# Optimization experiments

Measured on AMD Instinct MI355X. Metric: run time of the kernel, lower is better.

## Reference

```python
import jax, jax.numpy as jnp
import numpy as np

B, H, S, D, R = 2, 16, 2048, 64, 64  # batch, heads, seq, head_dim, R_features


def setup_inputs() -> dict:
    key = jax.random.key(0)
    ks = jax.random.split(key, 5)
    query = jax.random.normal(ks[0], (B, H, S, D), jnp.float32)
    keys = jax.random.normal(ks[1], (B, H, S, D), jnp.float32)
    vals = jax.random.normal(ks[2], (B, H, S, D), jnp.float32)
    # causal mask; masked_fill(mask == 0, -inf)
    mask = jnp.tril(jnp.ones((S, S), jnp.int32))[None, None]
    # LazyLinear(R) params: weight [D, R] (stored pre-transposed), bias [R]
    W = jax.random.normal(ks[3], (D, R), jnp.float32) / np.float32(np.sqrt(D))
    b = jax.random.normal(ks[4], (R,), jnp.float32) * 0.02
    return {"query": query, "keys": keys, "vals": vals, "mask": mask, "W": W, "b": b}


def reference(query, keys, vals, mask, W, b):
    d = query.shape[-1]
    r = W.shape[-1]
    # random-feature projections
    Wq = query @ W + b            # [B,H,S,R]
    Wk = keys @ W + b             # [B,H,S,R]
    phi_q = jnp.concatenate([jnp.cos(Wq), jnp.sin(Wq)], axis=-1)  # [B,H,S,2R]
    phi_k = jnp.concatenate([jnp.cos(Wk), jnp.sin(Wk)], axis=-1)
    energy = jnp.einsum("bhqr,bhkr->bhqk", phi_q, phi_k) / r      # [B,H,S,S]
    energy = energy * energy
    preattn = jnp.log(energy + 1e-5)
    # magnitude term: (||q||_2^2 + ||k||_2^2) / (2*sqrt(d))
    qn = jnp.sum(query * query, axis=-1, keepdims=True)           # [B,H,S,1]
    kn = jnp.sum(keys * keys, axis=-1, keepdims=True)             # [B,H,S,1]
    preattn = preattn + (qn + jnp.swapaxes(kn, -2, -1)) / (2.0 * d ** 0.5)
    preattn = jnp.where(mask == 0, -jnp.inf, preattn)
    attn = jax.nn.softmax(preattn, axis=-1)
    # dropout is identity in eval mode
    return attn @ vals  # [B,H,S,D]
```

## Files before the change

### kernel.cpp

```cpp
#include <hip/hip_runtime.h>
#include <hip/hip_fp16.h>

#define SEQ 2048
#define NBH 32
#define C1f 0.09016844005556021f

typedef _Float16 f16x8 __attribute__((ext_vector_type(8)));
typedef __fp16 fp16x2 __attribute__((ext_vector_type(2)));
typedef float f32x4 __attribute__((ext_vector_type(4)));
typedef __attribute__((address_space(1))) const unsigned GASU;
typedef __attribute__((address_space(3))) unsigned LASU;

union U16 { fp16x2 h[4]; f16x8 v; };

__device__ __forceinline__ void gll16(const void* g, void* l) {
  __builtin_amdgcn_global_load_lds((GASU*)g, (LASU*)l, 16, 0, 0);
}

__global__ __launch_bounds__(256) void prep(
    const float* __restrict__ qg, const float* __restrict__ kg,
    const float* __restrict__ vg, const float* __restrict__ Wg,
    const float* __restrict__ bg,
    __half* __restrict__ phiq, __half* __restrict__ phik,
    __half* __restrict__ vt, float* __restrict__ ckn) {
  __shared__ __align__(16) float smem[64 * 68 + 64 * 64];
  const int x = blockIdx.x;
  const int tid = threadIdx.x;
  if (x >= 2048) {
    const int i = x - 2048;
    const int bh = i >> 5, s0 = (i & 31) * 64;
    float* t = smem;
    const float* base = vg + ((long)bh * SEQ + s0) * 64;
    #pragma unroll
    for (int i2 = 0; i2 < 4; ++i2) {
      int seg = i2 * 256 + tid;
      int srow = seg >> 4, sc4 = (seg & 15) << 2;
      float4 xv = *(const float4*)(base + srow * 64 + sc4);
      t[srow * 65 + sc4 + 0] = xv.x; t[srow * 65 + sc4 + 1] = xv.y;
      t[srow * 65 + sc4 + 2] = xv.z; t[srow * 65 + sc4 + 3] = xv.w;
    }
    __syncthreads();
    int d = tid >> 2, sc = (tid & 3) << 4;
    __half tmp[16];
    #pragma unroll
    for (int j = 0; j < 16; ++j) tmp[j] = __float2half(t[(sc + j) * 65 + d]);
    __half* dst = vt + ((long)bh * 64 + d) * SEQ + s0 + sc;
    *(uint4*)dst = *(uint4*)&tmp[0];
    *(uint4*)(dst + 8) = *(uint4*)&tmp[8];
    return;
  }
  const int wave = tid >> 6, lane = tid & 63;
  const int g = lane >> 4, ql = lane & 15;
  const int isk = x >= 1024;
  const long rowblk = (long)(x & 1023) * 64;
  const float* src = isk ? kg : qg;
  __half* dphi = isk ? phik : phiq;
  float* w_l = smem;
  float* x_l = smem + 64 * 68;

  #pragma unroll
  for (int i2 = 0; i2 < 4; ++i2) {
    int seg = i2 * 256 + tid;
    int d = seg >> 4, rc = (seg & 15) << 2;
    float4 wv = *(const float4*)(Wg + d * 64 + rc);
    w_l[(rc + 0) * 68 + d] = wv.x; w_l[(rc + 1) * 68 + d] = wv.y;
    w_l[(rc + 2) * 68 + d] = wv.z; w_l[(rc + 3) * 68 + d] = wv.w;
  }
  const float* xb = src + rowblk * 64;
  #pragma unroll
  for (int i2 = 0; i2 < 4; ++i2) {
    int seg = i2 * 256 + tid;
    int row = seg >> 4;
    int off = ((seg & 15) * 4) ^ ((row & 7) << 2);
    gll16(xb + row * 64 + off, &x_l[seg * 4]);
  }
  float bias[4];
  #pragma unroll
  for (int rt = 0; rt < 4; ++rt) bias[rt] = bg[rt * 16 + ql];
  __syncthreads();

  f16x8 bh_[2][4], bl_[2][4];
  #pragma unroll
  for (int rt = 0; rt < 4; ++rt)
    #pragma unroll
    for (int ks = 0; ks < 2; ++ks) {
      f32x4 wa = *(const f32x4*)&w_l[(rt * 16 + ql) * 68 + ks * 32 + g * 8];
      f32x4 wb = *(const f32x4*)&w_l[(rt * 16 + ql) * 68 + ks * 32 + g * 8 + 4];
      #pragma unroll
      for (int j = 0; j < 4; ++j) {
        float w0 = wa[j]; _Float16 h0 = (_Float16)w0;
        bh_[ks][rt][j] = h0; bl_[ks][rt][j] = (_Float16)(w0 - (float)h0);
        float w1 = wb[j]; _Float16 h1 = (_Float16)w1;
        bh_[ks][rt][4 + j] = h1; bl_[ks][rt][4 + j] = (_Float16)(w1 - (float)h1);
      }
    }

  const int rl = wave * 16 + ql;
  float xv[16];
  #pragma unroll
  for (int ks = 0; ks < 2; ++ks)
    #pragma unroll
    for (int h = 0; h < 2; ++h) {
      int fi = (rl * 64 + ks * 32 + g * 8 + h * 4) ^ ((ql & 7) << 2);
      f32x4 u = *(const f32x4*)&x_l[fi];
      #pragma unroll
      for (int j = 0; j < 4; ++j) xv[ks * 8 + h * 4 + j] = u[j];
    }
  float nn = 0.f;
  #pragma unroll
  for (int j = 0; j < 16; ++j) nn = fmaf(xv[j], xv[j], nn);
  nn += __shfl_xor(nn, 16);
  nn += __shfl_xor(nn, 32);
  if (isk && g == 0) ckn[rowblk + rl] = 1e-5f * exp2f(nn * C1f);
  float scl = isk ? exp2f(nn * (C1f * 0.5f)) * 0.125f : 0.125f;
  float s4[4];
  #pragma unroll
  for (int i2 = 0; i2 < 4; ++i2) s4[i2] = __shfl(scl, (lane & 48) | (g * 4 + i2));

  f16x8 ah[2], al[2];
  #pragma unroll
  for (int ks = 0; ks < 2; ++ks)
    #pragma unroll
    for (int j = 0; j < 8; ++j) {
      float v = xv[ks * 8 + j];
      _Float16 hv = (_Float16)v;
      ah[ks][j] = hv;
      al[ks][j] = (_Float16)(v - (float)hv);
    }
  f32x4 sacc[4] = {};
  #pragma unroll
  for (int ks = 0; ks < 2; ++ks)
    #pragma unroll
    for (int rt = 0; rt < 4; ++rt) {
      sacc[rt] = __builtin_amdgcn_mfma_f32_16x16x32_f16(ah[ks], bh_[ks][rt], sacc[rt], 0, 0, 0);
      sacc[rt] = __builtin_amdgcn_mfma_f32_16x16x32_f16(al[ks], bh_[ks][rt], sacc[rt], 0, 0, 0);
      sacc[rt] = __builtin_amdgcn_mfma_f32_16x16x32_f16(ah[ks], bl_[ks][rt], sacc[rt], 0, 0, 0);
    }
  #pragma unroll
  for (int rt = 0; rt < 4; ++rt)
    #pragma unroll
    for (int i2 = 0; i2 < 4; ++i2) {
      float wq = sacc[rt][i2] + bias[rt];
      float sv, cv;
      __sincosf(wq, &sv, &cv);
      long row = rowblk + wave * 16 + g * 4 + i2;
      dphi[row * 128 + rt * 16 + ql] = __float2half(cv * s4[i2]);
      dphi[row * 128 + 64 + rt * 16 + ql] = __float2half(sv * s4[i2]);
    }
}

__global__ __launch_bounds__(256, 3) void attn_kernel(
    const __half* __restrict__ phiq_g, const __half* __restrict__ phik_g,
    const __half* __restrict__ vt_g, const float* __restrict__ ckn_g,
    float* __restrict__ out) {
  const int x = blockIdx.x;
  const int bh = ((x & 7) << 2) | ((x >> 3) & 3);
  const int u = (x >> 5) & 7;
  const int slot = x >> 8;
  const int s = (slot == 0) ? 31 - u : (slot == 1) ? 16 + u : (slot == 2) ? 15 - u : u;
  const int tid = threadIdx.x;
  const int wv = tid >> 6, lane = tid & 63;
  const int g = lane >> 4, ql = lane & 15;
  const int qh = wv & 1, kh = wv >> 1;
  const long rowbase = (long)bh * SEQ;
  const int qbase = s * 64 + qh * 32;

  __shared__ __align__(16) char smem[49152];
  __half* phik_l = (__half*)smem;
  __half* vt_l = (__half*)(smem + 32768);

  const __half* pkb = phik_g + rowbase * 128;
  const __half* vtb = vt_g + (long)bh * 64 * SEQ;
  const float* ckp = ckn_g + rowbase + kh * 32 + g * 8;

  unsigned koffv[4], kdstv[4], voffv[2], vdstv[2];
  #pragma unroll
  for (int i = 0; i < 4; ++i) {
    int seg = i * 256 + tid;
    int rho = seg >> 4;
    int sg = (rho & 32) | ((rho & 12) << 1) | ((rho & 16) >> 2) | (rho & 3);
    int off = ((seg & 15) * 8) ^ ((rho & 15) << 3);
    koffv[i] = sg * 128 + off;
    kdstv[i] = seg * 8;
  }
  #pragma unroll
  for (int i = 0; i < 2; ++i) {
    int seg = i * 256 + tid;
    int d = seg >> 3;
    int off = ((seg & 7) * 8) ^ ((d & 7) << 3);
    voffv[i] = d * SEQ + off;
    vdstv[i] = seg * 8;
  }

  auto stageKV = [&](int tn, int bb) {
    const __half* kb = pkb + (long)tn * 8192;
    #pragma unroll
    for (int i = 0; i < 4; ++i) gll16(kb + koffv[i], phik_l + bb * 8192 + kdstv[i]);
    const __half* vb = vtb + tn * 64;
    #pragma unroll
    for (int i = 0; i < 2; ++i) gll16(vb + voffv[i], vt_l + bb * 4096 + vdstv[i]);
  };

  stageKV(0, 0);

  f16x8 bq[2][4];
  #pragma unroll
  for (int c = 0; c < 2; ++c)
    #pragma unroll
    for (int ks = 0; ks < 4; ++ks)
      bq[c][ks] = *(const f16x8*)(phiq_g + (rowbase + qbase + c * 16 + ql) * 128 + ks * 32 + g * 8);

  float lsum[2] = {0.f, 0.f};
  f32x4 acc[2][4] = {};

  auto step = [&](int t, int bb) {
    asm volatile("s_waitcnt vmcnt(0)" ::: "memory");
    __builtin_amdgcn_s_barrier();
    __builtin_amdgcn_sched_barrier(0);

    const float* ckt = ckp + t * 64;
    f32x4 ckA = *(const f32x4*)(ckt);
    f32x4 ckB = *(const f32x4*)(ckt + 4);
    __builtin_amdgcn_sched_barrier(0);
    if (t < s) stageKV(t + 1, bb ^ 1);
    __builtin_amdgcn_sched_barrier(0);

    const bool skip = (qbase + 31) < (t * 64 + kh * 32);
    if (!skip) {
      f32x4 sS[2][2] = {};
      __builtin_amdgcn_s_setprio(1);
      #pragma unroll
      for (int ks = 0; ks < 4; ++ks) {
        int i0 = (bb * 8192 + (kh * 32 + ql) * 128 + ks * 32 + g * 8) ^ (ql << 3);
        int i1 = (bb * 8192 + (kh * 32 + 16 + ql) * 128 + ks * 32 + g * 8) ^ (ql << 3);
        f16x8 a0 = *(const f16x8*)&phik_l[i0];
        f16x8 a1 = *(const f16x8*)&phik_l[i1];
        sS[0][0] = __builtin_amdgcn_mfma_f32_16x16x32_f16(a0, bq[0][ks], sS[0][0], 0, 0, 0);
        sS[0][1] = __builtin_amdgcn_mfma_f32_16x16x32_f16(a1, bq[0][ks], sS[0][1], 0, 0, 0);
        sS[1][0] = __builtin_amdgcn_mfma_f32_16x16x32_f16(a0, bq[1][ks], sS[1][0], 0, 0, 0);
        sS[1][1] = __builtin_amdgcn_mfma_f32_16x16x32_f16(a1, bq[1][ks], sS[1][1], 0, 0, 0);
      }
      __builtin_amdgcn_s_setprio(0);

      f16x8 pa[2];
      #pragma unroll
      for (int c = 0; c < 2; ++c) {
        const int qrow = qbase + c * 16 + ql;
        const bool domask = (t * 64 + kh * 32 + 31) > (qbase + c * 16);
        float e[8];
        #pragma unroll
        for (int kt = 0; kt < 2; ++kt)
          #pragma unroll
          for (int r = 0; r < 4; ++r) {
            float dd = sS[c][kt][r];
            float pe = fmaf(dd, dd, kt ? ckB[r] : ckA[r]);
            if (domask) {
              int key = t * 64 + kh * 32 + g * 8 + kt * 4 + r;
              pe = (key <= qrow) ? pe : 0.f;
            }
            e[kt * 4 + r] = pe;
          }
        lsum[c] += ((e[0] + e[1]) + (e[2] + e[3])) + ((e[4] + e[5]) + (e[6] + e[7]));
        U16 A;
        A.h[0] = __builtin_amdgcn_cvt_pkrtz(e[0], e[1]);
        A.h[1] = __builtin_amdgcn_cvt_pkrtz(e[2], e[3]);
        A.h[2] = __builtin_amdgcn_cvt_pkrtz(e[4], e[5]);
        A.h[3] = __builtin_amdgcn_cvt_pkrtz(e[6], e[7]);
        pa[c] = A.v;
      }

      __builtin_amdgcn_s_setprio(1);
      #pragma unroll
      for (int dt = 0; dt < 4; ++dt) {
        int idx = (bb * 4096 + (dt * 16 + ql) * 64 + kh * 32 + g * 8) ^ ((ql & 7) << 3);
        f16x8 bv = *(const f16x8*)&vt_l[idx];
        acc[0][dt] = __builtin_amdgcn_mfma_f32_16x16x32_f16(pa[0], bv, acc[0][dt], 0, 0, 0);
        acc[1][dt] = __builtin_amdgcn_mfma_f32_16x16x32_f16(pa[1], bv, acc[1][dt], 0, 0, 0);
      }
      __builtin_amdgcn_s_setprio(0);
    }
  };

  for (int t = 0; t <= s; t += 2) {
    step(t, 0);
    if (t + 1 <= s) step(t + 1, 1);
  }

  float* dump = (float*)smem;
  __syncthreads();
  if (kh) {
    #pragma unroll
    for (int c = 0; c < 2; ++c) {
      #pragma unroll
      for (int dt = 0; dt < 4; ++dt)
        #pragma unroll
        for (int r = 0; r < 4; ++r)
          dump[(qh * 34 + c * 16 + dt * 4 + r) * 64 + lane] = acc[c][dt][r];
      dump[(qh * 34 + 32 + c) * 64 + lane] = lsum[c];
    }
  }
  __syncthreads();
  if (!kh) {
    #pragma unroll
    for (int c = 0; c < 2; ++c) {
      lsum[c] += dump[(qh * 34 + 32 + c) * 64 + lane];
      lsum[c] += __shfl_xor(lsum[c], 16);
      lsum[c] += __shfl_xor(lsum[c], 32);
      #pragma unroll
      for (int dt = 0; dt < 4; ++dt)
        #pragma unroll
        for (int r = 0; r < 4; ++r)
          acc[c][dt][r] += dump[(qh * 34 + c * 16 + dt * 4 + r) * 64 + lane];
    }
    #pragma unroll
    for (int c = 0; c < 2; ++c)
      #pragma unroll
      for (int r = 0; r < 4; ++r) {
        float ls = __shfl(lsum[c], (lane & 48) | (g * 4 + r));
        float inv = __builtin_amdgcn_rcpf(ls);
        float* o = out + (rowbase + qbase + c * 16 + g * 4 + r) * 64 + ql;
        #pragma unroll
        for (int dt = 0; dt < 4; ++dt) o[dt * 16] = acc[c][dt][r] * inv;
      }
  }
}

extern "C" void kernel_launch(void* const* d_in, const int* in_sizes, int n_in,
                              void* d_out, int out_size, void* d_ws, size_t ws_size,
                              hipStream_t stream) {
  const float* q = (const float*)d_in[0];
  const float* k = (const float*)d_in[1];
  const float* v = (const float*)d_in[2];
  const float* W = (const float*)d_in[4];
  const float* b = (const float*)d_in[5];
  float* out = (float*)d_out;

  char* ws = (char*)d_ws;
  __half* phiq = (__half*)ws;
  __half* phik = (__half*)(ws + 16777216);
  __half* vt = (__half*)(ws + 33554432);
  float* ckn = (float*)(ws + 41943040);

  prep<<<dim3(3072), 256, 0, stream>>>(q, k, v, W, b, phiq, phik, vt, ckn);
  attn_kernel<<<dim3(1024), 256, 0, stream>>>(phiq, phik, vt, ckn, out);
}
```

Baseline: 61.47 us.

## Compute query random features inside attention kernel instead of prep pass

Moves the phi_q projection (split-fp16 MFMA GEMM plus sincos) from the prep kernel into the attention kernel's prologue. The query tile is loaded into LDS and projected there, and the result is read back as MFMA operands. Prep now handles only keys, the V transpose, and one extra block that writes split-fp16 transposed W for the attention kernel to load. This removes the phi_q global write and re-read and cuts prep's block count. In exchange, the attention kernel gains a longer prologue with extra barriers and register pressure.

```diff
diff --git a/kernel.cpp b/kernel.cpp
--- a/kernel.cpp
+++ b/kernel.cpp
@@ -18,16 +18,30 @@
 }
 
 __global__ __launch_bounds__(256) void prep(
-    const float* __restrict__ qg, const float* __restrict__ kg,
-    const float* __restrict__ vg, const float* __restrict__ Wg,
-    const float* __restrict__ bg,
-    __half* __restrict__ phiq, __half* __restrict__ phik,
-    __half* __restrict__ vt, float* __restrict__ ckn) {
+    const float* __restrict__ kg, const float* __restrict__ vg,
+    const float* __restrict__ Wg, const float* __restrict__ bg,
+    __half* __restrict__ phik, __half* __restrict__ vt,
+    float* __restrict__ ckn, __half* __restrict__ wth, __half* __restrict__ wtl) {
   __shared__ __align__(16) float smem[64 * 68 + 64 * 64];
   const int x = blockIdx.x;
   const int tid = threadIdx.x;
-  if (x >= 2048) {
-    const int i = x - 2048;
+  if (x == 2048) {
+    int r = tid & 63, dg = tid >> 6;
+    __half th[16], tl[16];
+    #pragma unroll
+    for (int j = 0; j < 16; ++j) {
+      float w = Wg[(dg * 16 + j) * 64 + r];
+      th[j] = __float2half(w);
+      tl[j] = __float2half(w - __half2float(th[j]));
+    }
+    *(uint4*)&wth[r * 64 + dg * 16] = *(uint4*)&th[0];
+    *(uint4*)&wth[r * 64 + dg * 16 + 8] = *(uint4*)&th[8];
+    *(uint4*)&wtl[r * 64 + dg * 16] = *(uint4*)&tl[0];
+    *(uint4*)&wtl[r * 64 + dg * 16 + 8] = *(uint4*)&tl[8];
+    return;
+  }
+  if (x >= 1024) {
+    const int i = x - 1024;
     const int bh = i >> 5, s0 = (i & 31) * 64;
     float* t = smem;
     const float* base = vg + ((long)bh * SEQ + s0) * 64;
@@ -51,10 +65,7 @@
   }
   const int wave = tid >> 6, lane = tid & 63;
   const int g = lane >> 4, ql = lane & 15;
-  const int isk = x >= 1024;
-  const long rowblk = (long)(x & 1023) * 64;
-  const float* src = isk ? kg : qg;
-  __half* dphi = isk ? phik : phiq;
+  const long rowblk = (long)x * 64;
   float* w_l = smem;
   float* x_l = smem + 64 * 68;
 
@@ -66,7 +77,7 @@
     w_l[(rc + 0) * 68 + d] = wv.x; w_l[(rc + 1) * 68 + d] = wv.y;
     w_l[(rc + 2) * 68 + d] = wv.z; w_l[(rc + 3) * 68 + d] = wv.w;
   }
-  const float* xb = src + rowblk * 64;
+  const float* xb = kg + rowblk * 64;
   #pragma unroll
   for (int i2 = 0; i2 < 4; ++i2) {
     int seg = i2 * 256 + tid;
@@ -111,8 +122,8 @@
   for (int j = 0; j < 16; ++j) nn = fmaf(xv[j], xv[j], nn);
   nn += __shfl_xor(nn, 16);
   nn += __shfl_xor(nn, 32);
-  if (isk && g == 0) ckn[rowblk + rl] = 1e-5f * exp2f(nn * C1f);
-  float scl = isk ? exp2f(nn * (C1f * 0.5f)) * 0.125f : 0.125f;
+  if (g == 0) ckn[rowblk + rl] = 1e-5f * exp2f(nn * C1f);
+  float scl = exp2f(nn * (C1f * 0.5f)) * 0.125f;
   float s4[4];
   #pragma unroll
   for (int i2 = 0; i2 < 4; ++i2) s4[i2] = __shfl(scl, (lane & 48) | (g * 4 + i2));
@@ -144,15 +155,16 @@
       float sv, cv;
       __sincosf(wq, &sv, &cv);
       long row = rowblk + wave * 16 + g * 4 + i2;
-      dphi[row * 128 + rt * 16 + ql] = __float2half(cv * s4[i2]);
-      dphi[row * 128 + 64 + rt * 16 + ql] = __float2half(sv * s4[i2]);
+      phik[row * 128 + rt * 16 + ql] = __float2half(cv * s4[i2]);
+      phik[row * 128 + 64 + rt * 16 + ql] = __float2half(sv * s4[i2]);
     }
 }
 
 __global__ __launch_bounds__(256, 3) void attn_kernel(
-    const __half* __restrict__ phiq_g, const __half* __restrict__ phik_g,
+    const float* __restrict__ qg, const __half* __restrict__ phik_g,
     const __half* __restrict__ vt_g, const float* __restrict__ ckn_g,
-    float* __restrict__ out) {
+    const __half* __restrict__ wth, const __half* __restrict__ wtl,
+    const float* __restrict__ bg, float* __restrict__ out) {
   const int x = blockIdx.x;
   const int bh = ((x & 7) << 2) | ((x >> 3) & 3);
   const int u = (x >> 5) & 7;
@@ -173,6 +185,82 @@
   const __half* vtb = vt_g + (long)bh * 64 * SEQ;
   const float* ckp = ckn_g + rowbase + kh * 32 + g * 8;
 
+  f16x8 bq[2][4];
+  {
+    float* x_l = (float*)smem;
+    __half* phi_l = (__half*)smem + 8192;
+    const float* xb = qg + (rowbase + s * 64) * 64;
+    #pragma unroll
+    for (int i = 0; i < 4; ++i) {
+      int seg = i * 256 + tid;
+      int row = seg >> 4;
+      int off = ((seg & 15) * 4) ^ ((row & 7) << 2);
+      gll16(xb + row * 64 + off, &x_l[seg * 4]);
+    }
+    f16x8 bh_[2][4], bl_[2][4];
+    #pragma unroll
+    for (int rt = 0; rt < 4; ++rt)
+      #pragma unroll
+      for (int ks = 0; ks < 2; ++ks) {
+        bh_[ks][rt] = *(const f16x8*)&wth[(rt * 16 + ql) * 64 + ks * 32 + g * 8];
+        bl_[ks][rt] = *(const f16x8*)&wtl[(rt * 16 + ql) * 64 + ks * 32 + g * 8];
+      }
+    float bias[4];
+    #pragma unroll
+    for (int rt = 0; rt < 4; ++rt) bias[rt] = bg[rt * 16 + ql];
+    asm volatile("s_waitcnt vmcnt(0)" ::: "memory");
+    __builtin_amdgcn_s_barrier();
+
+    const int rl = wv * 16 + ql;
+    float xv[16];
+    #pragma unroll
+    for (int ks = 0; ks < 2; ++ks)
+      #pragma unroll
+      for (int h = 0; h < 2; ++h) {
+        int fi = (rl * 64 + ks * 32 + g * 8 + h * 4) ^ ((ql & 7) << 2);
+        f32x4 uu = *(const f32x4*)&x_l[fi];
+        #pragma unroll
+        for (int j = 0; j < 4; ++j) xv[ks * 8 + h * 4 + j] = uu[j];
+      }
+    f16x8 ah[2], al[2];
+    #pragma unroll
+    for (int ks = 0; ks < 2; ++ks)
+      #pragma unroll
+      for (int j = 0; j < 8; ++j) {
+        float v = xv[ks * 8 + j];
+        _Float16 hv = (_Float16)v;
+        ah[ks][j] = hv;
+        al[ks][j] = (_Float16)(v - (float)hv);
+      }
+    f32x4 sacc[4] = {};
+    #pragma unroll
+    for (int ks = 0; ks < 2; ++ks)
+      #pragma unroll
+      for (int rt = 0; rt < 4; ++rt) {
+        sacc[rt] = __builtin_amdgcn_mfma_f32_16x16x32_f16(ah[ks], bh_[ks][rt], sacc[rt], 0, 0, 0);
+        sacc[rt] = __builtin_amdgcn_mfma_f32_16x16x32_f16(al[ks], bh_[ks][rt], sacc[rt], 0, 0, 0);
+        sacc[rt] = __builtin_amdgcn_mfma_f32_16x16x32_f16(ah[ks], bl_[ks][rt], sacc[rt], 0, 0, 0);
+      }
+    #pragma unroll
+    for (int rt = 0; rt < 4; ++rt)
+      #pragma unroll
+      for (int i2 = 0; i2 < 4; ++i2) {
+        float wq = sacc[rt][i2] + bias[rt];
+        float sv, cv;
+        __sincosf(wq, &sv, &cv);
+        int row = wv * 16 + g * 4 + i2;
+        phi_l[row * 128 + rt * 16 + ql] = __float2half(cv * 0.125f);
+        phi_l[row * 128 + 64 + rt * 16 + ql] = __float2half(sv * 0.125f);
+      }
+    __syncthreads();
+    #pragma unroll
+    for (int c = 0; c < 2; ++c)
+      #pragma unroll
+      for (int ks = 0; ks < 4; ++ks)
+        bq[c][ks] = *(const f16x8*)&phi_l[(qh * 32 + c * 16 + ql) * 128 + ks * 32 + g * 8];
+    __syncthreads();
+  }
+
   unsigned koffv[4], kdstv[4], voffv[2], vdstv[2];
   #pragma unroll
   for (int i = 0; i < 4; ++i) {
@@ -202,13 +290,6 @@
   };
 
   stageKV(0, 0);
-
-  f16x8 bq[2][4];
-  #pragma unroll
-  for (int c = 0; c < 2; ++c)
-    #pragma unroll
-    for (int ks = 0; ks < 4; ++ks)
-      bq[c][ks] = *(const f16x8*)(phiq_g + (rowbase + qbase + c * 16 + ql) * 128 + ks * 32 + g * 8);
 
   float lsum[2] = {0.f, 0.f};
   f32x4 acc[2][4] = {};
@@ -336,11 +417,12 @@
   float* out = (float*)d_out;
 
   char* ws = (char*)d_ws;
-  __half* phiq = (__half*)ws;
   __half* phik = (__half*)(ws + 16777216);
   __half* vt = (__half*)(ws + 33554432);
   float* ckn = (float*)(ws + 41943040);
-
-  prep<<<dim3(3072), 256, 0, stream>>>(q, k, v, W, b, phiq, phik, vt, ckn);
-  attn_kernel<<<dim3(1024), 256, 0, stream>>>(phiq, phik, vt, ckn, out);
+  __half* wth = (__half*)(ws + 41943040 + 262144);
+  __half* wtl = wth + 64 * 64;
+
+  prep<<<dim3(2049), 256, 0, stream>>>(k, v, W, b, phik, vt, ckn, wth, wtl);
+  attn_kernel<<<dim3(1024), 256, 0, stream>>>(q, phik, vt, ckn, wth, wtl, b, out);
 }
```

Result: slower. 64.04 us (+4.2%).
